# Kernel optimization log

Hardware: AMD Instinct MI355X
Metric: run time of the kernel (lower is better)

## Reference

```python
import jax, jax.numpy as jnp
import numpy as np

B, N, P, H, BINF = 64, 100, 640000, 128, 11

def setup_inputs() -> dict:
    key = jax.random.key(0)
    ks = jax.random.split(key, 10)
    s = 1.0 / np.sqrt(H)
    sparse_idx = jnp.stack([
        jax.random.randint(ks[0], (P,), 0, B),
        jax.random.randint(ks[1], (P,), 0, N),
        jax.random.randint(ks[2], (P,), 0, N),
    ], axis=1).astype(jnp.int64)  # [P, 3]
    return {
        "local_pair": jax.random.normal(ks[3], (P, H), jnp.float32),
        "global_pair": jax.random.normal(ks[4], (P, H), jnp.float32),
        "binary": jax.random.normal(ks[5], (B, N, N, BINF), jnp.float32),
        "sparse_idx": sparse_idx,
        "W_local": jax.random.normal(ks[6], (H, H), jnp.float32) * s,
        "W_global": jax.random.normal(ks[7], (H, H), jnp.float32) * s,
        "b_global": jnp.zeros((H,), jnp.float32),
        "W_binary": jax.random.normal(ks[8], (BINF, H), jnp.float32) * s,
        "W_score": jax.random.normal(ks[9], (H, 5), jnp.float32) * s,
        "b_score": jnp.zeros((5,), jnp.float32),
    }

def reference(local_pair, global_pair, binary, sparse_idx,
              W_local, W_global, b_global, W_binary, W_score, b_score):
    # gather binary bond features for each scored pair: [P, BINF]
    binary_feats = binary[sparse_idx[:, 0], sparse_idx[:, 1], sparse_idx[:, 2]]
    # fused 3-way linear + relu
    pair_feats = jax.nn.relu(
        local_pair @ W_local
        + (global_pair @ W_global + b_global)
        + binary_feats @ W_binary
    )  # [P, H]
    score = pair_feats @ W_score + b_score  # [P, 5]
    return score
```

## Files before the change

kernel.cpp:

```cpp
#include <hip/hip_runtime.h>
#include <stdint.h>

typedef __bf16 bf16x8 __attribute__((ext_vector_type(8)));
typedef float f32x16 __attribute__((ext_vector_type(16)));

#define H 128
#define NBINF 11
#define NCHUNK 17
#define PTOT 640000
#define ROWS 32
#define NT (PTOT / ROWS)
#define GRID 512
#define ASTRIDE 560
#define ABUF (ROWS * ASTRIDE)
#define FSTRIDE 272
#define PARTOFF 9216

__device__ __align__(16) unsigned short g_wpack[NCHUNK * 4 * 64 * 8];
__device__ __align__(16) unsigned short g_wsp[8 * 64 * 8];
__device__ int g_flag;

__device__ __forceinline__ unsigned short f2bf(float f) {
  return (unsigned short)__builtin_bit_cast(unsigned short, (__bf16)f);
}

__global__ void k_flag(const int* __restrict__ sidx) {
  int t = threadIdx.x;
  int v = sidx[2 * t + 1];
  unsigned long long any = __ballot(v != 0);
  if (t == 0) g_flag = (any == 0ull) ? 2 : 1;
}

__global__ void k_pack(const float* __restrict__ Wl, const float* __restrict__ Wg,
                       const float* __restrict__ Wb, const float* __restrict__ Wsc) {
  int tid = blockIdx.x * 256 + threadIdx.x;
  if (tid < NCHUNK * 4 * 64 * 8) {
    int j = tid & 7, l = (tid >> 3) & 63, nt = (tid >> 9) & 3, c = tid >> 11;
    int k = c * 16 + ((l >> 5) << 3) + j;
    int n = nt * 32 + (l & 31);
    float v = 0.f;
    if (k < 128)       v = Wl[k * H + n];
    else if (k < 256)  v = Wg[(k - 128) * H + n];
    else { int kk = k - 256; v = (kk < NBINF) ? Wb[kk * H + n] : 0.f; }
    g_wpack[tid] = f2bf(v);
  }
  if (tid < 8 * 64 * 8) {
    int j = tid & 7, l = (tid >> 3) & 63, cs = tid >> 9;
    int s = l & 31;
    int k = cs * 16 + ((l >> 5) << 3) + j;
    float v = (s < 5) ? Wsc[k * 5 + s] : 0.f;
    g_wsp[tid] = f2bf(v);
  }
}

__device__ __forceinline__ void bar_lgkm() {
  asm volatile("s_waitcnt lgkmcnt(0)" ::: "memory");
  __builtin_amdgcn_s_barrier();
}

__launch_bounds__(256, 2)
__global__ void k_main(const float* __restrict__ lp, const float* __restrict__ gp,
                       const float* __restrict__ bin, const int* __restrict__ sidx,
                       const float* __restrict__ bg, const float* __restrict__ bsc,
                       float* __restrict__ out) {
  __shared__ __align__(16) char sm[2 * ABUF];
  const int t   = threadIdx.x;
  const int wid = t >> 6;
  const int l   = t & 63;
  const int lr  = l & 31;
  const int lh  = l >> 5;
  const int sflag = g_flag;

  bf16x8 wreg[NCHUNK];
#pragma unroll
  for (int c = 0; c < NCHUNK; ++c)
    wreg[c] = *(const bf16x8*)(g_wpack + ((size_t)(c * 4 + wid) * 64 + l) * 8);
  bf16x8 ws0 = *(const bf16x8*)(g_wsp + ((size_t)(2 * wid + 0) * 64 + l) * 8);
  bf16x8 ws1 = *(const bf16x8*)(g_wsp + ((size_t)(2 * wid + 1) * 64 + l) * 8);

  const float bgv = bg[wid * 32 + lr];

  float4 payA[8]; float bvA[8];
  float4 payB[8]; float bvB[8];

  auto issue = [&](int tile, float4 (&pay)[8], float (&bv)[8]) {
    const int p0 = tile * ROWS;
#pragma unroll
    for (int i = 0; i < 4; ++i) {
      int v = t + 256 * i;
      int row = v >> 5, c32 = v & 31;
      const float* src = (c32 < 16)
          ? lp + (size_t)(p0 + row) * H + c32 * 8
          : gp + (size_t)(p0 + row) * H + (c32 - 16) * 8;
      pay[2 * i]     = ((const float4*)src)[0];
      pay[2 * i + 1] = ((const float4*)src)[1];
    }
    if (t < 2 * ROWS) {
      int row = t >> 1, bh = t & 1, prow = p0 + row;
      int bi = sidx[(prow * 3 + 0) * sflag];
      int ii = sidx[(prow * 3 + 1) * sflag];
      int jj = sidx[(prow * 3 + 2) * sflag];
      int base = ((bi * 100 + ii) * 100 + jj) * NBINF;
#pragma unroll
      for (int j = 0; j < 8; ++j) {
        int e = bh * 8 + j;
        bv[j] = (e < NBINF) ? bin[base + e] : 0.f;
      }
    }
  };

  auto commit = [&](char* dst, float4 (&pay)[8], float (&bv)[8]) {
#pragma unroll
    for (int i = 0; i < 4; ++i) {
      int v = t + 256 * i;
      int row = v >> 5, c32 = v & 31;
      float4 a = pay[2 * i], b = pay[2 * i + 1];
      bf16x8 x;
      x[0] = (__bf16)a.x; x[1] = (__bf16)a.y; x[2] = (__bf16)a.z; x[3] = (__bf16)a.w;
      x[4] = (__bf16)b.x; x[5] = (__bf16)b.y; x[6] = (__bf16)b.z; x[7] = (__bf16)b.w;
      *(bf16x8*)(dst + row * ASTRIDE + c32 * 16) = x;
    }
    if (t < 2 * ROWS) {
      int row = t >> 1, bh = t & 1;
      bf16x8 x;
#pragma unroll
      for (int j = 0; j < 8; ++j) x[j] = (__bf16)bv[j];
      *(bf16x8*)(dst + row * ASTRIDE + 512 + bh * 16) = x;
    }
  };

  auto compute = [&](char* buf, int tile) {
    f32x16 acc = {};
#pragma unroll
    for (int c = 0; c < NCHUNK; ++c) {
      bf16x8 a = *(const bf16x8*)(buf + lr * ASTRIDE + c * 32 + lh * 16);
      acc = __builtin_amdgcn_mfma_f32_32x32x16_bf16(a, wreg[c], acc, 0, 0, 0);
    }
    bar_lgkm();
#pragma unroll
    for (int rg = 0; rg < 16; ++rg) {
      int p = (rg & 3) + ((rg >> 2) << 3) + (lh << 2);
      float fv = fmaxf(acc[rg] + bgv, 0.f);
      *(__bf16*)(buf + (size_t)p * FSTRIDE + (size_t)(wid * 32 + lr) * 2) = (__bf16)fv;
    }
    bar_lgkm();
    f32x16 sacc = {};
    bf16x8 fb0 = *(const bf16x8*)(buf + (size_t)lr * FSTRIDE + (2 * wid) * 32 + lh * 16);
    bf16x8 fb1 = *(const bf16x8*)(buf + (size_t)lr * FSTRIDE + (2 * wid + 1) * 32 + lh * 16);
    sacc = __builtin_amdgcn_mfma_f32_32x32x16_bf16(ws0, fb0, sacc, 0, 0, 0);
    sacc = __builtin_amdgcn_mfma_f32_32x32x16_bf16(ws1, fb1, sacc, 0, 0, 0);
    char* part = buf + PARTOFF;
    if (lh == 0) {
#pragma unroll
      for (int s = 0; s < 4; ++s)
        *(float*)(part + ((size_t)(s * 32 + lr) * 4 + wid) * 4) = sacc[s];
    } else {
      *(float*)(part + ((size_t)(4 * 32 + lr) * 4 + wid) * 4) = sacc[0];
    }
    bar_lgkm();
    if (t < 160) {
      int s = t >> 5, p = t & 31;
      float4 q = *(const float4*)(part + (size_t)t * 16);
      out[(size_t)(tile * ROWS + p) * 5 + s] = q.x + q.y + q.z + q.w + bsc[s];
    }
  };

  const int t0 = blockIdx.x;
  issue(t0, payA, bvA);
  commit(sm, payA, bvA);
  issue(t0 + GRID, payB, bvB);
  bar_lgkm();

  for (int u = t0; u < NT; u += 2 * GRID) {
    const int v = u + GRID;
    if (u + 2 * GRID < NT) issue(u + 2 * GRID, payA, bvA);
    compute(sm, u);
    if (v < NT) commit(sm + ABUF, payB, bvB);
    bar_lgkm();
    if (v < NT) {
      if (v + 2 * GRID < NT) issue(v + 2 * GRID, payB, bvB);
      compute(sm + ABUF, v);
      if (u + 2 * GRID < NT) commit(sm, payA, bvA);
      bar_lgkm();
    }
  }
}

extern "C" void kernel_launch(void* const* d_in, const int* in_sizes, int n_in,
                              void* d_out, int out_size, void* d_ws, size_t ws_size,
                              hipStream_t stream) {
  const float* lp  = (const float*)d_in[0];
  const float* gp  = (const float*)d_in[1];
  const float* bin = (const float*)d_in[2];
  const int*   si  = (const int*)d_in[3];
  const float* Wl  = (const float*)d_in[4];
  const float* Wg  = (const float*)d_in[5];
  const float* bg  = (const float*)d_in[6];
  const float* Wb  = (const float*)d_in[7];
  const float* Wsc = (const float*)d_in[8];
  const float* bsc = (const float*)d_in[9];
  float* out = (float*)d_out;

  hipLaunchKernelGGL(k_flag, dim3(1), dim3(64), 0, stream, si);
  hipLaunchKernelGGL(k_pack, dim3(136), dim3(256), 0, stream, Wl, Wg, Wb, Wsc);
  hipLaunchKernelGGL(k_main, dim3(GRID), dim3(256), 0, stream,
                     lp, gp, bin, si, bg, bsc, out);
}
```

Measured before the change: 162.8 us.

## Cut register prefetch depth to one tile and raise occupancy to three blocks

Replaces the two in-flight register payload sets with a single prefetch buffer, leaving a simple double-buffered LDS loop. This frees registers so launch bounds can allow three blocks per CU, and the grid grows to match. It also spreads the binary gather over 128 threads, caches the score bias in a register and changes the partial-sum layout in LDS. The cost is less load lookahead per block, which now relies on extra resident blocks to hide memory latency.

```diff
diff --git a/kernel.cpp b/kernel.cpp
--- a/kernel.cpp
+++ b/kernel.cpp
@@ -2,6 +2,7 @@
 #include <stdint.h>
 
 typedef __bf16 bf16x8 __attribute__((ext_vector_type(8)));
+typedef __bf16 bf16x4 __attribute__((ext_vector_type(4)));
 typedef float f32x16 __attribute__((ext_vector_type(16)));
 
 #define H 128
@@ -10,7 +11,7 @@
 #define PTOT 640000
 #define ROWS 32
 #define NT (PTOT / ROWS)
-#define GRID 512
+#define GRID 768
 #define ASTRIDE 560
 #define ABUF (ROWS * ASTRIDE)
 #define FSTRIDE 272
@@ -58,7 +59,7 @@
   __builtin_amdgcn_s_barrier();
 }
 
-__launch_bounds__(256, 2)
+__launch_bounds__(256, 3)
 __global__ void k_main(const float* __restrict__ lp, const float* __restrict__ gp,
                        const float* __restrict__ bin, const int* __restrict__ sidx,
                        const float* __restrict__ bg, const float* __restrict__ bsc,
@@ -79,11 +80,12 @@
   bf16x8 ws1 = *(const bf16x8*)(g_wsp + ((size_t)(2 * wid + 1) * 64 + l) * 8);
 
   const float bgv = bg[wid * 32 + lr];
-
-  float4 payA[8]; float bvA[8];
-  float4 payB[8]; float bvB[8];
-
-  auto issue = [&](int tile, float4 (&pay)[8], float (&bv)[8]) {
+  const float bscv = (t < 160) ? bsc[t >> 5] : 0.f;
+
+  float4 pay[8];
+  float  bv[4];
+
+  auto issue = [&](int tile) {
     const int p0 = tile * ROWS;
 #pragma unroll
     for (int i = 0; i < 4; ++i) {
@@ -95,21 +97,21 @@
       pay[2 * i]     = ((const float4*)src)[0];
       pay[2 * i + 1] = ((const float4*)src)[1];
     }
-    if (t < 2 * ROWS) {
-      int row = t >> 1, bh = t & 1, prow = p0 + row;
+    if (t < 4 * ROWS) {
+      int row = t >> 2, q = t & 3, prow = p0 + row;
       int bi = sidx[(prow * 3 + 0) * sflag];
       int ii = sidx[(prow * 3 + 1) * sflag];
       int jj = sidx[(prow * 3 + 2) * sflag];
       int base = ((bi * 100 + ii) * 100 + jj) * NBINF;
 #pragma unroll
-      for (int j = 0; j < 8; ++j) {
-        int e = bh * 8 + j;
+      for (int j = 0; j < 4; ++j) {
+        int e = 4 * q + j;
         bv[j] = (e < NBINF) ? bin[base + e] : 0.f;
       }
     }
   };
 
-  auto commit = [&](char* dst, float4 (&pay)[8], float (&bv)[8]) {
+  auto commit = [&](char* dst) {
 #pragma unroll
     for (int i = 0; i < 4; ++i) {
       int v = t + 256 * i;
@@ -120,12 +122,12 @@
       x[4] = (__bf16)b.x; x[5] = (__bf16)b.y; x[6] = (__bf16)b.z; x[7] = (__bf16)b.w;
       *(bf16x8*)(dst + row * ASTRIDE + c32 * 16) = x;
     }
-    if (t < 2 * ROWS) {
-      int row = t >> 1, bh = t & 1;
-      bf16x8 x;
-#pragma unroll
-      for (int j = 0; j < 8; ++j) x[j] = (__bf16)bv[j];
-      *(bf16x8*)(dst + row * ASTRIDE + 512 + bh * 16) = x;
+    if (t < 4 * ROWS) {
+      int row = t >> 2, q = t & 3;
+      bf16x4 x;
+#pragma unroll
+      for (int j = 0; j < 4; ++j) x[j] = (__bf16)bv[j];
+      *(bf16x4*)(dst + row * ASTRIDE + 512 + q * 8) = x;
     }
   };
 
@@ -149,40 +151,34 @@
     bf16x8 fb1 = *(const bf16x8*)(buf + (size_t)lr * FSTRIDE + (2 * wid + 1) * 32 + lh * 16);
     sacc = __builtin_amdgcn_mfma_f32_32x32x16_bf16(ws0, fb0, sacc, 0, 0, 0);
     sacc = __builtin_amdgcn_mfma_f32_32x32x16_bf16(ws1, fb1, sacc, 0, 0, 0);
-    char* part = buf + PARTOFF;
+    float* part = (float*)(buf + PARTOFF);
     if (lh == 0) {
 #pragma unroll
       for (int s = 0; s < 4; ++s)
-        *(float*)(part + ((size_t)(s * 32 + lr) * 4 + wid) * 4) = sacc[s];
+        part[wid * 160 + s * 32 + lr] = sacc[s];
     } else {
-      *(float*)(part + ((size_t)(4 * 32 + lr) * 4 + wid) * 4) = sacc[0];
+      part[wid * 160 + 128 + lr] = sacc[0];
     }
     bar_lgkm();
     if (t < 160) {
-      int s = t >> 5, p = t & 31;
-      float4 q = *(const float4*)(part + (size_t)t * 16);
-      out[(size_t)(tile * ROWS + p) * 5 + s] = q.x + q.y + q.z + q.w + bsc[s];
+      float r = part[t] + part[160 + t] + part[320 + t] + part[480 + t];
+      out[(size_t)(tile * ROWS + (t & 31)) * 5 + (t >> 5)] = r + bscv;
     }
   };
 
   const int t0 = blockIdx.x;
-  issue(t0, payA, bvA);
-  commit(sm, payA, bvA);
-  issue(t0 + GRID, payB, bvB);
+  issue(t0);
+  commit(sm);
   bar_lgkm();
 
-  for (int u = t0; u < NT; u += 2 * GRID) {
-    const int v = u + GRID;
-    if (u + 2 * GRID < NT) issue(u + 2 * GRID, payA, bvA);
-    compute(sm, u);
-    if (v < NT) commit(sm + ABUF, payB, bvB);
-    bar_lgkm();
-    if (v < NT) {
-      if (v + 2 * GRID < NT) issue(v + 2 * GRID, payB, bvB);
-      compute(sm + ABUF, v);
-      if (u + 2 * GRID < NT) commit(sm, payA, bvA);
-      bar_lgkm();
-    }
+  int cur = 0;
+  for (int u = t0; u < NT; u += GRID) {
+    const int nxt = u + GRID;
+    if (nxt < NT) issue(nxt);
+    compute(sm + cur * ABUF, u);
+    if (nxt < NT) commit(sm + (cur ^ 1) * ABUF);
+    bar_lgkm();
+    cur ^= 1;
   }
 }
 
```

New measurement: 144.3 us. -11.4%, faster.
